# Performance work log

Hardware: AMD Instinct MI355X
Metric: run time of the kernel (lower is better)

## Reference

```python
import jax, jax.numpy as jnp
import numpy as np

N_NODES = 50000
N_EDGES = 800000
IN_DIM = 128
HIDDEN = 16
HEADS1 = 8
OUT_DIM = 128
NEG_SLOPE = 0.2
EPS = 1e-16


def gat_conv(x, src, dst, W, att_src, att_dst, bias, heads, out_ch, concat, num_nodes):
    # x: [N, F_in]; W: [F_in, heads*out_ch]; att_*: [heads, out_ch]; bias: [heads*out_ch] or [out_ch]
    h = (x @ W).reshape(num_nodes, heads, out_ch)          # [N, H, C]
    a_src = jnp.einsum('nhc,hc->nh', h, att_src)           # [N, H]
    a_dst = jnp.einsum('nhc,hc->nh', h, att_dst)           # [N, H]
    alpha = a_src[src] + a_dst[dst]                        # [E, H]
    alpha = jax.nn.leaky_relu(alpha, NEG_SLOPE)
    # segment softmax over incoming edges of each dst node
    amax = jax.ops.segment_max(alpha, dst, num_segments=num_nodes)  # [N, H]
    e = jnp.exp(alpha - amax[dst])                         # [E, H]
    denom = jax.ops.segment_sum(e, dst, num_segments=num_nodes)     # [N, H]
    alpha = e / (denom[dst] + EPS)                         # [E, H]
    msg = h[src] * alpha[:, :, None]                       # [E, H, C]
    out = jax.ops.segment_sum(msg, dst, num_segments=num_nodes)     # [N, H, C]
    if concat:
        out = out.reshape(num_nodes, heads * out_ch)
    else:
        out = out.mean(axis=1)
    return out + bias


def setup_inputs() -> dict:
    key = jax.random.key(0)
    ks = jax.random.split(key, 12)
    x = jax.random.normal(ks[0], (N_NODES, IN_DIM), dtype=jnp.float32)
    edge_index = jax.random.randint(ks[1], (2, N_EDGES), 0, N_NODES, dtype=jnp.int32)
    s1 = 1.0 / np.sqrt(IN_DIM)
    s2 = 1.0 / np.sqrt(HIDDEN * HEADS1)
    W1 = jax.random.normal(ks[2], (IN_DIM, HEADS1 * HIDDEN), dtype=jnp.float32) * s1
    att_src1 = jax.random.normal(ks[3], (HEADS1, HIDDEN), dtype=jnp.float32) * s1
    att_dst1 = jax.random.normal(ks[4], (HEADS1, HIDDEN), dtype=jnp.float32) * s1
    bias1 = jnp.zeros((HEADS1 * HIDDEN,), dtype=jnp.float32)
    W2 = jax.random.normal(ks[5], (HEADS1 * HIDDEN, OUT_DIM), dtype=jnp.float32) * s2
    att_src2 = jax.random.normal(ks[6], (1, OUT_DIM), dtype=jnp.float32) * s2
    att_dst2 = jax.random.normal(ks[7], (1, OUT_DIM), dtype=jnp.float32) * s2
    bias2 = jnp.zeros((OUT_DIM,), dtype=jnp.float32)
    return {"x": x, "edge_index": edge_index,
            "W1": W1, "att_src1": att_src1, "att_dst1": att_dst1, "bias1": bias1,
            "W2": W2, "att_src2": att_src2, "att_dst2": att_dst2, "bias2": bias2}


def reference(x, edge_index, W1, att_src1, att_dst1, bias1, W2, att_src2, att_dst2, bias2):
    # eval mode: F.dropout and attention dropout are identity
    src, dst = edge_index[0], edge_index[1]
    h = gat_conv(x, src, dst, W1, att_src1, att_dst1, bias1,
                 HEADS1, HIDDEN, True, N_NODES)            # [N, HEADS1*HIDDEN]
    h = jax.nn.elu(h)
    out = gat_conv(h, src, dst, W2, att_src2, att_dst2, bias2,
                   1, OUT_DIM, False, N_NODES)             # [N, OUT_DIM]
    return out
```

## Files before the change

### kernel.cpp

```cpp
#include <hip/hip_runtime.h>

#define N_NODES 50000
#define N_EDGES 800000
#define CAP 64
#define NBUCK 196
#define NODES_PAD 50176
#define BBLK 256
#define EPB 3125
#define LOG2E 1.4426950408889634f

typedef unsigned int uint;
typedef unsigned short ushort;
typedef __attribute__((ext_vector_type(2))) float f32x2;
typedef __attribute__((ext_vector_type(4))) float f32x4;
typedef __attribute__((ext_vector_type(8))) short s16x8;

__device__ __forceinline__ f32x2 pk_add(f32x2 a, f32x2 b) {
    f32x2 d;
    asm("v_pk_add_f32 %0, %1, %2" : "=v"(d) : "v"(a), "v"(b));
    return d;
}
__device__ __forceinline__ f32x2 pk_mul(f32x2 a, f32x2 b) {
    f32x2 d;
    asm("v_pk_mul_f32 %0, %1, %2" : "=v"(d) : "v"(a), "v"(b));
    return d;
}
__device__ __forceinline__ f32x2 pk_fma(f32x2 a, f32x2 b, f32x2 c) {
    f32x2 d;
    asm("v_pk_fma_f32 %0, %1, %2, %3" : "=v"(d) : "v"(a), "v"(b), "v"(c));
    return d;
}

__device__ __forceinline__ ushort f2bf(float f) {
    uint u = __float_as_uint(f);
    u = (u + 0x7fffu + ((u >> 16) & 1u)) >> 16;
    return (ushort)u;
}
__device__ __forceinline__ float bf_lo(uint u) { return __uint_as_float(u << 16); }
__device__ __forceinline__ float bf_hi(uint u) { return __uint_as_float(u & 0xffff0000u); }

__global__ __launch_bounds__(256) void bin_count_kernel(
    const int* __restrict__ dstv, uint* __restrict__ counts)
{
    __shared__ uint hist[NBUCK];
    int tid = threadIdx.x, b = blockIdx.x;
    for (int k = tid; k < NBUCK; k += 256) hist[k] = 0;
    __syncthreads();
    int e0 = b * EPB;
    for (int i = tid; i < EPB; i += 256)
        atomicAdd(&hist[((uint)dstv[e0 + i]) >> 8], 1u);
    __syncthreads();
    for (int k = tid; k < NBUCK; k += 256) counts[k * BBLK + b] = hist[k];
}

__global__ __launch_bounds__(256) void scan1_kernel(
    const uint* __restrict__ counts, uint* __restrict__ ofs, uint* __restrict__ bsum)
{
    __shared__ uint wtot[4];
    int tid = threadIdx.x, k = blockIdx.x;
    int lane = tid & 63, wid = tid >> 6;
    uint v = counts[k * 256 + tid];
    uint inc = v;
    #pragma unroll
    for (int o = 1; o < 64; o <<= 1) {
        uint t = __shfl_up(inc, o);
        if (lane >= o) inc += t;
    }
    if (lane == 63) wtot[wid] = inc;
    __syncthreads();
    uint woff = 0;
    for (int w = 0; w < wid; w++) woff += wtot[w];
    uint excl = woff + inc - v;
    ofs[k * 256 + tid] = excl;
    if (tid == 255) bsum[k] = excl + v;
}

__global__ __launch_bounds__(64) void scan2_kernel(
    const uint* __restrict__ bsum, uint* __restrict__ bbase)
{
    int lane = threadIdx.x;
    int base = lane * 4;
    uint v[4];
    #pragma unroll
    for (int j = 0; j < 4; j++) v[j] = (base + j < NBUCK) ? bsum[base + j] : 0u;
    uint s = v[0] + v[1] + v[2] + v[3];
    uint inc = s;
    #pragma unroll
    for (int o = 1; o < 64; o <<= 1) {
        uint t = __shfl_up(inc, o);
        if (lane >= o) inc += t;
    }
    uint run = inc - s;
    #pragma unroll
    for (int j = 0; j < 4; j++) {
        if (base + j < NBUCK) { bbase[base + j] = run; run += v[j]; }
    }
}

__global__ __launch_bounds__(256) void bin_scatter_kernel(
    const int* __restrict__ srcv, const int* __restrict__ dstv,
    const uint* __restrict__ ofs, const uint* __restrict__ bbase,
    uint* __restrict__ binned)
{
    __shared__ uint cur[NBUCK];
    int tid = threadIdx.x, b = blockIdx.x;
    for (int k = tid; k < NBUCK; k += 256) cur[k] = ofs[k * BBLK + b] + bbase[k];
    __syncthreads();
    int e0 = b * EPB;
    for (int i = tid; i < EPB; i += 256) {
        int d = dstv[e0 + i], s = srcv[e0 + i];
        uint k = ((uint)d) >> 8;
        uint pos = atomicAdd(&cur[k], 1u);
        binned[pos] = (((uint)d & 255u) << 16) | (uint)s;
    }
}

__global__ __launch_bounds__(256) void build_kernel(
    const uint* __restrict__ binned, const uint* __restrict__ ofs,
    const uint* __restrict__ bbase,
    int* __restrict__ deg, ushort* __restrict__ list)
{
    __shared__ uint ldeg[256];
    __shared__ ushort llist[256 * CAP];
    int tid = threadIdx.x, k = blockIdx.x;
    ldeg[tid] = 0;
    __syncthreads();
    uint start = ofs[k * 256] + bbase[k];
    uint end = (k == NBUCK - 1) ? N_EDGES : (ofs[(k + 1) * 256] + bbase[k + 1]);
    for (uint i = start + tid; i < end; i += 256) {
        uint p = binned[i];
        uint nl = (p >> 16) & 255u;
        uint slot = atomicAdd(&ldeg[nl], 1u);
        if (slot < CAP) llist[(nl << 6) + slot] = (ushort)(p & 0xFFFFu);
    }
    __syncthreads();
    int node0 = k << 8;
    deg[node0 + tid] = (int)ldeg[tid];
    uint4* d4 = (uint4*)(list + (size_t)node0 * CAP);
    const uint4* s4 = (const uint4*)llist;
    for (int i = tid; i < 256 * CAP * 2 / 16; i += 256) d4[i] = s4[i];
}

__global__ __launch_bounds__(256) void prep_kernel(
    const float* __restrict__ W1, const float* __restrict__ as1, const float* __restrict__ ad1,
    const float* __restrict__ W2, const float* __restrict__ as2, const float* __restrict__ ad2,
    float* __restrict__ WS1, float* __restrict__ WS2)
{
    int idx = blockIdx.x * 256 + threadIdx.x;
    if (idx < 2048) {
        int k = idx >> 4, j = idx & 15;
        const float* att = (j < 8) ? as1 : ad1;
        int head = j & 7;
        float s = 0.f;
        #pragma unroll
        for (int c = 0; c < 16; c++)
            s += W1[k * 128 + head * 16 + c] * att[head * 16 + c];
        WS1[idx] = s * LOG2E;
    } else if (idx < 4096) {
        int idx2 = idx - 2048;
        int k = idx2 >> 4, j = idx2 & 15;
        float s = 0.f;
        if (j < 2) {
            const float* att = j ? ad2 : as2;
            for (int c = 0; c < 128; c++) s += W2[k * 128 + c] * att[c];
        }
        WS2[idx2] = s * LOG2E;
    }
}

template <int HEADS, bool ABF16>
__global__ __launch_bounds__(512) void gemm_mfma_kernel(
    const void* __restrict__ Av, const float* __restrict__ W,
    const float* __restrict__ WS,
    ushort* __restrict__ h16, float* __restrict__ a_src, float* __restrict__ a_dst,
    int nrows)
{
    __shared__ ushort Bf[2304 * 8];
    int tid = threadIdx.x;
    for (int idx = tid; idx < 2304; idx += 512) {
        int t = idx >> 8;
        int rem = idx & 255;
        int kt = rem >> 6, L = rem & 63;
        int col = L & 15;
        int kb = ((L >> 4) << 3) + (kt << 5);
        ushort tmp[8];
        if (t < 8) {
            #pragma unroll
            for (int j = 0; j < 8; j++)
                tmp[j] = f2bf(W[(size_t)(kb + j) * 128 + (t << 4) + col]);
        } else {
            #pragma unroll
            for (int j = 0; j < 8; j++)
                tmp[j] = f2bf(WS[(kb + j) * 16 + col]);
        }
        uint p0 = (uint)tmp[0] | ((uint)tmp[1] << 16);
        uint p1 = (uint)tmp[2] | ((uint)tmp[3] << 16);
        uint p2 = (uint)tmp[4] | ((uint)tmp[5] << 16);
        uint p3 = (uint)tmp[6] | ((uint)tmp[7] << 16);
        *(uint4*)&Bf[idx * 8] = make_uint4(p0, p1, p2, p3);
    }
    __syncthreads();

    int lane = tid & 63;
    int wv = tid >> 6;
    int row0 = (blockIdx.x * 8 + wv) * 16;
    if (row0 >= nrows) return;

    int m = lane & 15, kg = lane >> 4;
    s16x8 afrag[4];
    if (ABF16) {
        const ushort* arow = (const ushort*)Av + (size_t)(row0 + m) * 128 + (kg << 3);
        #pragma unroll
        for (int kt = 0; kt < 4; kt++)
            afrag[kt] = *(const s16x8*)(arow + (kt << 5));
    } else {
        const float* arow = (const float*)Av + (size_t)(row0 + m) * 128 + (kg << 3);
        #pragma unroll
        for (int kt = 0; kt < 4; kt++) {
            float4 f0 = *(const float4*)(arow + (kt << 5));
            float4 f1 = *(const float4*)(arow + (kt << 5) + 4);
            union { s16x8 v; ushort us[8]; } uu;
            uu.us[0] = f2bf(f0.x); uu.us[1] = f2bf(f0.y);
            uu.us[2] = f2bf(f0.z); uu.us[3] = f2bf(f0.w);
            uu.us[4] = f2bf(f1.x); uu.us[5] = f2bf(f1.y);
            uu.us[6] = f2bf(f1.z); uu.us[7] = f2bf(f1.w);
            afrag[kt] = uu.v;
        }
    }

    f32x4 acc[9];
    #pragma unroll
    for (int t = 0; t < 9; t++) acc[t] = (f32x4){0.f, 0.f, 0.f, 0.f};
    #pragma unroll
    for (int t = 0; t < 9; t++) {
        #pragma unroll
        for (int kt = 0; kt < 4; kt++) {
            s16x8 b = *(const s16x8*)&Bf[(((t << 2) + kt) * 64 + lane) * 8];
            acc[t] = __builtin_amdgcn_mfma_f32_16x16x32_bf16(afrag[kt], b, acc[t], 0, 0, 0);
        }
    }

    int colw = lane & 15;
    int rbase = row0 + ((lane >> 4) << 2);
    #pragma unroll
    for (int t = 0; t < 8; t++) {
        #pragma unroll
        for (int r = 0; r < 4; r++)
            h16[(size_t)(rbase + r) * 128 + (t << 4) + colw] = f2bf(acc[t][r]);
    }
    #pragma unroll
    for (int r = 0; r < 4; r++) {
        float v = acc[8][r];
        int row = rbase + r;
        if (HEADS == 8) {
            if (colw < 8) a_src[row * 8 + colw] = v;
            else          a_dst[row * 8 + (colw - 8)] = v;
        } else {
            if (colw == 0)      a_src[row] = v;
            else if (colw == 1) a_dst[row] = v;
        }
    }
}

template <int HEADS, bool ELU, bool OUT16>
__global__ __launch_bounds__(256) void agg_kernel(
    const ushort* __restrict__ h16, const ushort* __restrict__ list,
    const int* __restrict__ deg,
    const float* __restrict__ a_src, const float* __restrict__ a_dst,
    const float* __restrict__ bias, void* __restrict__ outv)
{
    __shared__ float w_lds[4][HEADS][65];
    __shared__ int s_lds[4][64];
    __shared__ float sh_l[4][8];
    int lane = threadIdx.x & 63;
    int wv = threadIdx.x >> 6;
    int n = blockIdx.x * 4 + wv;
    int d = min(deg[n], CAP);
    bool valid = lane < d;
    int s = valid ? (int)list[n * CAP + lane] : 0;
    s_lds[wv][lane] = s << 8;

    if (HEADS == 8) {
        float4 u0 = *(const float4*)&a_src[s * 8];
        float4 u1 = *(const float4*)&a_src[s * 8 + 4];
        float4 v0 = *(const float4*)&a_dst[n * 8];
        float4 v1 = *(const float4*)&a_dst[n * 8 + 4];
        float al[8] = {u0.x + v0.x, u0.y + v0.y, u0.z + v0.z, u0.w + v0.w,
                       u1.x + v1.x, u1.y + v1.y, u1.z + v1.z, u1.w + v1.w};
        float eh[8];
        #pragma unroll
        for (int hh = 0; hh < 8; hh++) {
            float a = fmaxf(al[hh], 0.2f * al[hh]);
            eh[hh] = valid ? exp2f(a) : 0.f;
            w_lds[wv][hh][lane] = eh[hh];
        }
        f32x2 s01 = {eh[0], eh[1]}, s23 = {eh[2], eh[3]};
        f32x2 s45 = {eh[4], eh[5]}, s67 = {eh[6], eh[7]};
        auto lvl = [&](int mm) {
            f32x2 t;
            t.x = __shfl_xor(s01.x, mm); t.y = __shfl_xor(s01.y, mm); s01 = pk_add(s01, t);
            t.x = __shfl_xor(s23.x, mm); t.y = __shfl_xor(s23.y, mm); s23 = pk_add(s23, t);
            t.x = __shfl_xor(s45.x, mm); t.y = __shfl_xor(s45.y, mm); s45 = pk_add(s45, t);
            t.x = __shfl_xor(s67.x, mm); t.y = __shfl_xor(s67.y, mm); s67 = pk_add(s67, t);
        };
        lvl(1); lvl(2); lvl(4); lvl(8);
        if (d > 16) lvl(16);
        if (d > 32) lvl(32);
        if (lane == 0) {
            *(f32x2*)&sh_l[wv][0] = s01; *(f32x2*)&sh_l[wv][2] = s23;
            *(f32x2*)&sh_l[wv][4] = s45; *(f32x2*)&sh_l[wv][6] = s67;
        }
    } else {
        float a = a_src[s] + a_dst[n];
        a = fmaxf(a, 0.2f * a);
        float eh0 = valid ? exp2f(a) : 0.f;
        w_lds[wv][0][lane] = eh0;
        float sh = eh0;
        sh += __shfl_xor(sh, 1); sh += __shfl_xor(sh, 2);
        sh += __shfl_xor(sh, 4); sh += __shfl_xor(sh, 8);
        if (d > 16) sh += __shfl_xor(sh, 16);
        if (d > 32) sh += __shfl_xor(sh, 32);
        if (lane == 0) sh_l[wv][0] = sh;
    }

    int half = lane >> 5;
    int lq = lane & 31;
    int c0 = lq << 2;
    int g = (HEADS == 8) ? (lq >> 2) : 0;
    const char* hp = (const char*)h16 + (c0 << 1);
    f32x2 acc01 = {0.f, 0.f}, acc23 = {0.f, 0.f};
    int d8 = (d + 7) & ~7;
    for (int e0 = 0; e0 < d8; e0 += 8) {
        int soff[4]; float wv4[4]; uint2 u[4];
        #pragma unroll
        for (int r = 0; r < 4; r++) {
            int e = e0 + (r << 1) + half;
            soff[r] = s_lds[wv][e];
            wv4[r] = w_lds[wv][g][e];
        }
        #pragma unroll
        for (int r = 0; r < 4; r++)
            u[r] = *(const uint2*)(hp + soff[r]);
        #pragma unroll
        for (int r = 0; r < 4; r++) {
            f32x2 wp = {wv4[r], wv4[r]};
            f32x2 lo = {bf_lo(u[r].x), bf_hi(u[r].x)};
            f32x2 hi = {bf_lo(u[r].y), bf_hi(u[r].y)};
            acc01 = pk_fma(wp, lo, acc01);
            acc23 = pk_fma(wp, hi, acc23);
        }
    }
    f32x2 t;
    t.x = __shfl_xor(acc01.x, 32); t.y = __shfl_xor(acc01.y, 32); acc01 = pk_add(acc01, t);
    t.x = __shfl_xor(acc23.x, 32); t.y = __shfl_xor(acc23.y, 32); acc23 = pk_add(acc23, t);

    float shv = sh_l[wv][g];
    float r = __builtin_amdgcn_rcpf(shv + 1e-16f);
    f32x2 rr = {r, r};
    acc01 = pk_mul(acc01, rr);
    acc23 = pk_mul(acc23, rr);
    float4 bv = *(const float4*)&bias[c0];
    float o0 = acc01.x + bv.x, o1 = acc01.y + bv.y;
    float o2 = acc23.x + bv.z, o3 = acc23.y + bv.w;
    if (ELU) {
        o0 = o0 > 0.f ? o0 : __expf(o0) - 1.f;
        o1 = o1 > 0.f ? o1 : __expf(o1) - 1.f;
        o2 = o2 > 0.f ? o2 : __expf(o2) - 1.f;
        o3 = o3 > 0.f ? o3 : __expf(o3) - 1.f;
    }
    if (lane < 32) {
        if (OUT16) {
            uint2 pk;
            pk.x = (uint)f2bf(o0) | ((uint)f2bf(o1) << 16);
            pk.y = (uint)f2bf(o2) | ((uint)f2bf(o3) << 16);
            *(uint2*)((ushort*)outv + (size_t)n * 128 + c0) = pk;
        } else {
            *(float4*)((float*)outv + (size_t)n * 128 + c0) = make_float4(o0, o1, o2, o3);
        }
    }
}

extern "C" void kernel_launch(void* const* d_in, const int* in_sizes, int n_in,
                              void* d_out, int out_size, void* d_ws, size_t ws_size,
                              hipStream_t stream)
{
    (void)in_sizes; (void)n_in; (void)out_size; (void)ws_size;
    const float* x   = (const float*)d_in[0];
    const int*   ei  = (const int*)d_in[1];
    const float* W1  = (const float*)d_in[2];
    const float* as1 = (const float*)d_in[3];
    const float* ad1 = (const float*)d_in[4];
    const float* b1  = (const float*)d_in[5];
    const float* W2  = (const float*)d_in[6];
    const float* as2 = (const float*)d_in[7];
    const float* ad2 = (const float*)d_in[8];
    const float* b2  = (const float*)d_in[9];
    float* out = (float*)d_out;
    const int* srcv = ei;
    const int* dstv = ei + N_EDGES;

    char* ws = (char*)d_ws;
    size_t off = 0;
    auto alloc = [&](size_t bytes) {
        void* p = ws + off;
        off += (bytes + 255) & ~(size_t)255;
        return p;
    };
    ushort* h1_16 = (ushort*)alloc((size_t)N_NODES * 128 * 2);
    ushort* h2_16 = (ushort*)alloc((size_t)N_NODES * 128 * 2);
    ushort* h1b   = (ushort*)alloc((size_t)N_NODES * 128 * 2);
    float*  asrc1 = (float*)alloc((size_t)N_NODES * 8 * 4);
    float*  adst1 = (float*)alloc((size_t)N_NODES * 8 * 4);
    float*  asrc2 = (float*)alloc((size_t)N_NODES * 4);
    float*  adst2 = (float*)alloc((size_t)N_NODES * 4);
    int*    degp  = (int*)alloc((size_t)NODES_PAD * 4);
    ushort* list  = (ushort*)alloc((size_t)NODES_PAD * CAP * 2);
    float*  WS1   = (float*)alloc(128 * 16 * 4);
    float*  WS2   = (float*)alloc(128 * 16 * 4);
    uint* binned = (uint*)h1b;
    uint* counts = binned + N_EDGES;
    uint* ofsp   = counts + NODES_PAD;
    uint* bsum   = ofsp + NODES_PAD;
    uint* bbase  = bsum + NBUCK;

    const int NG = (N_NODES + 3) / 4;
    const int GB = (N_NODES / 16 + 7) / 8;

    prep_kernel<<<16, 256, 0, stream>>>(W1, as1, ad1, W2, as2, ad2, WS1, WS2);
    bin_count_kernel<<<BBLK, 256, 0, stream>>>(dstv, counts);
    scan1_kernel<<<NBUCK, 256, 0, stream>>>(counts, ofsp, bsum);
    scan2_kernel<<<1, 64, 0, stream>>>(bsum, bbase);
    bin_scatter_kernel<<<BBLK, 256, 0, stream>>>(srcv, dstv, ofsp, bbase, binned);
    build_kernel<<<NBUCK, 256, 0, stream>>>(binned, ofsp, bbase, degp, list);

    gemm_mfma_kernel<8, false><<<GB, 512, 0, stream>>>(x, W1, WS1, h1_16, asrc1, adst1, N_NODES);
    agg_kernel<8, true, true><<<NG, 256, 0, stream>>>(h1_16, list, degp, asrc1, adst1, b1, h1b);

    gemm_mfma_kernel<1, true><<<GB, 512, 0, stream>>>(h1b, W2, WS2, h2_16, asrc2, adst2, N_NODES);
    agg_kernel<1, false, false><<<NG, 256, 0, stream>>>(h2_16, list, degp, asrc2, adst2, b2, out);
}
```

Before: 125.5 us.

## Split aggregation across channel groups, shrink build buckets, merge prep into scan2

The aggregation kernel now launches four blocks per node group, each handling 32 channels (two heads), and normalizes attention weights before accumulation. This spreads the gather work over more waves and trims the LDS per-head weight table. Binning now uses 64-node buckets (782 of them) so each build block needs less LDS and more blocks run in parallel. The prep kernel is folded into the scan2 launch to save one launch. More blocks re-read the neighbor lists and attention logits, and there are more scan1 blocks. With N_NODES/4*4 blocks the last grid covers exactly 50000 nodes.

```diff
diff --git a/kernel.cpp b/kernel.cpp
--- a/kernel.cpp
+++ b/kernel.cpp
@@ -3,8 +3,8 @@
 #define N_NODES 50000
 #define N_EDGES 800000
 #define CAP 64
-#define NBUCK 196
-#define NODES_PAD 50176
+#define NBUCK 782
+#define NODES_PAD 50048
 #define BBLK 256
 #define EPB 3125
 #define LOG2E 1.4426950408889634f
@@ -20,11 +20,6 @@
     asm("v_pk_add_f32 %0, %1, %2" : "=v"(d) : "v"(a), "v"(b));
     return d;
 }
-__device__ __forceinline__ f32x2 pk_mul(f32x2 a, f32x2 b) {
-    f32x2 d;
-    asm("v_pk_mul_f32 %0, %1, %2" : "=v"(d) : "v"(a), "v"(b));
-    return d;
-}
 __device__ __forceinline__ f32x2 pk_fma(f32x2 a, f32x2 b, f32x2 c) {
     f32x2 d;
     asm("v_pk_fma_f32 %0, %1, %2, %3" : "=v"(d) : "v"(a), "v"(b), "v"(c));
@@ -48,7 +43,7 @@
     __syncthreads();
     int e0 = b * EPB;
     for (int i = tid; i < EPB; i += 256)
-        atomicAdd(&hist[((uint)dstv[e0 + i]) >> 8], 1u);
+        atomicAdd(&hist[((uint)dstv[e0 + i]) >> 6], 1u);
     __syncthreads();
     for (int k = tid; k < NBUCK; k += 256) counts[k * BBLK + b] = hist[k];
 }
@@ -75,25 +70,58 @@
     if (tid == 255) bsum[k] = excl + v;
 }
 
-__global__ __launch_bounds__(64) void scan2_kernel(
-    const uint* __restrict__ bsum, uint* __restrict__ bbase)
-{
-    int lane = threadIdx.x;
-    int base = lane * 4;
-    uint v[4];
-    #pragma unroll
-    for (int j = 0; j < 4; j++) v[j] = (base + j < NBUCK) ? bsum[base + j] : 0u;
-    uint s = v[0] + v[1] + v[2] + v[3];
-    uint inc = s;
-    #pragma unroll
-    for (int o = 1; o < 64; o <<= 1) {
-        uint t = __shfl_up(inc, o);
-        if (lane >= o) inc += t;
-    }
-    uint run = inc - s;
-    #pragma unroll
-    for (int j = 0; j < 4; j++) {
-        if (base + j < NBUCK) { bbase[base + j] = run; run += v[j]; }
+__global__ __launch_bounds__(256) void scan2_prep_kernel(
+    const uint* __restrict__ bsum, uint* __restrict__ bbase,
+    const float* __restrict__ W1, const float* __restrict__ as1, const float* __restrict__ ad1,
+    const float* __restrict__ W2, const float* __restrict__ as2, const float* __restrict__ ad2,
+    float* __restrict__ WS1, float* __restrict__ WS2)
+{
+    int bid = blockIdx.x;
+    int tid = threadIdx.x;
+    if (bid == 0) {
+        __shared__ uint wtot[4];
+        int lane = tid & 63, wid = tid >> 6;
+        int base = tid * 4;
+        uint v[4];
+        #pragma unroll
+        for (int j = 0; j < 4; j++) v[j] = (base + j < NBUCK) ? bsum[base + j] : 0u;
+        uint s = v[0] + v[1] + v[2] + v[3];
+        uint inc = s;
+        #pragma unroll
+        for (int o = 1; o < 64; o <<= 1) {
+            uint t = __shfl_up(inc, o);
+            if (lane >= o) inc += t;
+        }
+        if (lane == 63) wtot[wid] = inc;
+        __syncthreads();
+        uint woff = 0;
+        for (int w = 0; w < wid; w++) woff += wtot[w];
+        uint run = woff + inc - s;
+        #pragma unroll
+        for (int j = 0; j < 4; j++) {
+            if (base + j < NBUCK) { bbase[base + j] = run; run += v[j]; }
+        }
+    } else {
+        int idx = (bid - 1) * 256 + tid;
+        if (idx < 2048) {
+            int k = idx >> 4, j = idx & 15;
+            const float* att = (j < 8) ? as1 : ad1;
+            int head = j & 7;
+            float s = 0.f;
+            #pragma unroll
+            for (int c = 0; c < 16; c++)
+                s += W1[k * 128 + head * 16 + c] * att[head * 16 + c];
+            WS1[idx] = s * LOG2E;
+        } else {
+            int idx2 = idx - 2048;
+            int k = idx2 >> 4, j = idx2 & 15;
+            float s = 0.f;
+            if (j < 2) {
+                const float* att = j ? ad2 : as2;
+                for (int c = 0; c < 128; c++) s += W2[k * 128 + c] * att[c];
+            }
+            WS2[idx2] = s * LOG2E;
+        }
     }
 }
 
@@ -109,9 +137,9 @@
     int e0 = b * EPB;
     for (int i = tid; i < EPB; i += 256) {
         int d = dstv[e0 + i], s = srcv[e0 + i];
-        uint k = ((uint)d) >> 8;
+        uint k = ((uint)d) >> 6;
         uint pos = atomicAdd(&cur[k], 1u);
-        binned[pos] = (((uint)d & 255u) << 16) | (uint)s;
+        binned[pos] = (((uint)d & 63u) << 16) | (uint)s;
     }
 }
 
@@ -120,52 +148,25 @@
     const uint* __restrict__ bbase,
     int* __restrict__ deg, ushort* __restrict__ list)
 {
-    __shared__ uint ldeg[256];
-    __shared__ ushort llist[256 * CAP];
+    __shared__ uint ldeg[64];
+    __shared__ ushort llist[64 * CAP];
     int tid = threadIdx.x, k = blockIdx.x;
-    ldeg[tid] = 0;
+    if (tid < 64) ldeg[tid] = 0;
     __syncthreads();
     uint start = ofs[k * 256] + bbase[k];
     uint end = (k == NBUCK - 1) ? N_EDGES : (ofs[(k + 1) * 256] + bbase[k + 1]);
     for (uint i = start + tid; i < end; i += 256) {
         uint p = binned[i];
-        uint nl = (p >> 16) & 255u;
+        uint nl = (p >> 16) & 63u;
         uint slot = atomicAdd(&ldeg[nl], 1u);
         if (slot < CAP) llist[(nl << 6) + slot] = (ushort)(p & 0xFFFFu);
     }
     __syncthreads();
-    int node0 = k << 8;
-    deg[node0 + tid] = (int)ldeg[tid];
+    int node0 = k << 6;
+    if (tid < 64) deg[node0 + tid] = (int)ldeg[tid];
     uint4* d4 = (uint4*)(list + (size_t)node0 * CAP);
     const uint4* s4 = (const uint4*)llist;
-    for (int i = tid; i < 256 * CAP * 2 / 16; i += 256) d4[i] = s4[i];
-}
-
-__global__ __launch_bounds__(256) void prep_kernel(
-    const float* __restrict__ W1, const float* __restrict__ as1, const float* __restrict__ ad1,
-    const float* __restrict__ W2, const float* __restrict__ as2, const float* __restrict__ ad2,
-    float* __restrict__ WS1, float* __restrict__ WS2)
-{
-    int idx = blockIdx.x * 256 + threadIdx.x;
-    if (idx < 2048) {
-        int k = idx >> 4, j = idx & 15;
-        const float* att = (j < 8) ? as1 : ad1;
-        int head = j & 7;
-        float s = 0.f;
-        #pragma unroll
-        for (int c = 0; c < 16; c++)
-            s += W1[k * 128 + head * 16 + c] * att[head * 16 + c];
-        WS1[idx] = s * LOG2E;
-    } else if (idx < 4096) {
-        int idx2 = idx - 2048;
-        int k = idx2 >> 4, j = idx2 & 15;
-        float s = 0.f;
-        if (j < 2) {
-            const float* att = j ? ad2 : as2;
-            for (int c = 0; c < 128; c++) s += W2[k * 128 + c] * att[c];
-        }
-        WS2[idx2] = s * LOG2E;
-    }
+    for (int i = tid; i < 64 * CAP * 2 / 16; i += 256) d4[i] = s4[i];
 }
 
 template <int HEADS, bool ABF16>
@@ -269,113 +270,99 @@
     const float* __restrict__ a_src, const float* __restrict__ a_dst,
     const float* __restrict__ bias, void* __restrict__ outv)
 {
-    __shared__ float w_lds[4][HEADS][65];
+    __shared__ float w_lds[4][2][64];
     __shared__ int s_lds[4][64];
-    __shared__ float sh_l[4][8];
+    int bid = blockIdx.x;
+    int cg = bid & 3;
     int lane = threadIdx.x & 63;
     int wv = threadIdx.x >> 6;
-    int n = blockIdx.x * 4 + wv;
+    int n = (bid >> 2) * 4 + wv;
     int d = min(deg[n], CAP);
     bool valid = lane < d;
     int s = valid ? (int)list[n * CAP + lane] : 0;
-    s_lds[wv][lane] = s << 8;
+    s_lds[wv][lane] = (s << 8) + (cg << 6);
 
     if (HEADS == 8) {
-        float4 u0 = *(const float4*)&a_src[s * 8];
-        float4 u1 = *(const float4*)&a_src[s * 8 + 4];
-        float4 v0 = *(const float4*)&a_dst[n * 8];
-        float4 v1 = *(const float4*)&a_dst[n * 8 + 4];
-        float al[8] = {u0.x + v0.x, u0.y + v0.y, u0.z + v0.z, u0.w + v0.w,
-                       u1.x + v1.x, u1.y + v1.y, u1.z + v1.z, u1.w + v1.w};
-        float eh[8];
-        #pragma unroll
-        for (int hh = 0; hh < 8; hh++) {
-            float a = fmaxf(al[hh], 0.2f * al[hh]);
-            eh[hh] = valid ? exp2f(a) : 0.f;
-            w_lds[wv][hh][lane] = eh[hh];
-        }
-        f32x2 s01 = {eh[0], eh[1]}, s23 = {eh[2], eh[3]};
-        f32x2 s45 = {eh[4], eh[5]}, s67 = {eh[6], eh[7]};
-        auto lvl = [&](int mm) {
-            f32x2 t;
-            t.x = __shfl_xor(s01.x, mm); t.y = __shfl_xor(s01.y, mm); s01 = pk_add(s01, t);
-            t.x = __shfl_xor(s23.x, mm); t.y = __shfl_xor(s23.y, mm); s23 = pk_add(s23, t);
-            t.x = __shfl_xor(s45.x, mm); t.y = __shfl_xor(s45.y, mm); s45 = pk_add(s45, t);
-            t.x = __shfl_xor(s67.x, mm); t.y = __shfl_xor(s67.y, mm); s67 = pk_add(s67, t);
-        };
-        lvl(1); lvl(2); lvl(4); lvl(8);
-        if (d > 16) lvl(16);
-        if (d > 32) lvl(32);
-        if (lane == 0) {
-            *(f32x2*)&sh_l[wv][0] = s01; *(f32x2*)&sh_l[wv][2] = s23;
-            *(f32x2*)&sh_l[wv][4] = s45; *(f32x2*)&sh_l[wv][6] = s67;
-        }
+        float2 us = *(const float2*)&a_src[s * 8 + 2 * cg];
+        float2 ud = *(const float2*)&a_dst[n * 8 + 2 * cg];
+        float a0 = us.x + ud.x, a1 = us.y + ud.y;
+        a0 = fmaxf(a0, 0.2f * a0);
+        a1 = fmaxf(a1, 0.2f * a1);
+        float e0 = valid ? exp2f(a0) : 0.f;
+        float e1 = valid ? exp2f(a1) : 0.f;
+        f32x2 ss = {e0, e1};
+        #pragma unroll
+        for (int mm = 1; mm < 16; mm <<= 1) {
+            f32x2 t; t.x = __shfl_xor(ss.x, mm); t.y = __shfl_xor(ss.y, mm);
+            ss = pk_add(ss, t);
+        }
+        if (d > 16) { f32x2 t; t.x = __shfl_xor(ss.x, 16); t.y = __shfl_xor(ss.y, 16); ss = pk_add(ss, t); }
+        if (d > 32) { f32x2 t; t.x = __shfl_xor(ss.x, 32); t.y = __shfl_xor(ss.y, 32); ss = pk_add(ss, t); }
+        w_lds[wv][0][lane] = e0 * __builtin_amdgcn_rcpf(ss.x + 1e-16f);
+        w_lds[wv][1][lane] = e1 * __builtin_amdgcn_rcpf(ss.y + 1e-16f);
     } else {
         float a = a_src[s] + a_dst[n];
         a = fmaxf(a, 0.2f * a);
-        float eh0 = valid ? exp2f(a) : 0.f;
-        w_lds[wv][0][lane] = eh0;
-        float sh = eh0;
+        float e0 = valid ? exp2f(a) : 0.f;
+        float sh = e0;
         sh += __shfl_xor(sh, 1); sh += __shfl_xor(sh, 2);
         sh += __shfl_xor(sh, 4); sh += __shfl_xor(sh, 8);
         if (d > 16) sh += __shfl_xor(sh, 16);
         if (d > 32) sh += __shfl_xor(sh, 32);
-        if (lane == 0) sh_l[wv][0] = sh;
-    }
-
-    int half = lane >> 5;
-    int lq = lane & 31;
-    int c0 = lq << 2;
-    int g = (HEADS == 8) ? (lq >> 2) : 0;
-    const char* hp = (const char*)h16 + (c0 << 1);
+        float w = e0 * __builtin_amdgcn_rcpf(sh + 1e-16f);
+        w_lds[wv][0][lane] = w;
+        w_lds[wv][1][lane] = w;
+    }
+
+    int eg = lane >> 3;
+    int lq = lane & 7;
+    int hsel = lq >> 2;
+    const char* hp = (const char*)h16 + (lq << 3);
+    uint2 u[8];
+    float wk[8];
+    #pragma unroll
+    for (int t = 0; t < 8; t++) {
+        if ((t << 3) < d) {
+            int e = (t << 3) + eg;
+            u[t] = *(const uint2*)(hp + s_lds[wv][e]);
+            wk[t] = w_lds[wv][hsel][e];
+        }
+    }
     f32x2 acc01 = {0.f, 0.f}, acc23 = {0.f, 0.f};
-    int d8 = (d + 7) & ~7;
-    for (int e0 = 0; e0 < d8; e0 += 8) {
-        int soff[4]; float wv4[4]; uint2 u[4];
-        #pragma unroll
-        for (int r = 0; r < 4; r++) {
-            int e = e0 + (r << 1) + half;
-            soff[r] = s_lds[wv][e];
-            wv4[r] = w_lds[wv][g][e];
-        }
-        #pragma unroll
-        for (int r = 0; r < 4; r++)
-            u[r] = *(const uint2*)(hp + soff[r]);
-        #pragma unroll
-        for (int r = 0; r < 4; r++) {
-            f32x2 wp = {wv4[r], wv4[r]};
-            f32x2 lo = {bf_lo(u[r].x), bf_hi(u[r].x)};
-            f32x2 hi = {bf_lo(u[r].y), bf_hi(u[r].y)};
+    #pragma unroll
+    for (int t = 0; t < 8; t++) {
+        if ((t << 3) < d) {
+            f32x2 wp = {wk[t], wk[t]};
+            f32x2 lo = {bf_lo(u[t].x), bf_hi(u[t].x)};
+            f32x2 hi = {bf_lo(u[t].y), bf_hi(u[t].y)};
             acc01 = pk_fma(wp, lo, acc01);
             acc23 = pk_fma(wp, hi, acc23);
         }
     }
-    f32x2 t;
-    t.x = __shfl_xor(acc01.x, 32); t.y = __shfl_xor(acc01.y, 32); acc01 = pk_add(acc01, t);
-    t.x = __shfl_xor(acc23.x, 32); t.y = __shfl_xor(acc23.y, 32); acc23 = pk_add(acc23, t);
-
-    float shv = sh_l[wv][g];
-    float r = __builtin_amdgcn_rcpf(shv + 1e-16f);
-    f32x2 rr = {r, r};
-    acc01 = pk_mul(acc01, rr);
-    acc23 = pk_mul(acc23, rr);
-    float4 bv = *(const float4*)&bias[c0];
-    float o0 = acc01.x + bv.x, o1 = acc01.y + bv.y;
-    float o2 = acc23.x + bv.z, o3 = acc23.y + bv.w;
-    if (ELU) {
-        o0 = o0 > 0.f ? o0 : __expf(o0) - 1.f;
-        o1 = o1 > 0.f ? o1 : __expf(o1) - 1.f;
-        o2 = o2 > 0.f ? o2 : __expf(o2) - 1.f;
-        o3 = o3 > 0.f ? o3 : __expf(o3) - 1.f;
-    }
-    if (lane < 32) {
+    #pragma unroll
+    for (int mm = 8; mm < 64; mm <<= 1) {
+        f32x2 t;
+        t.x = __shfl_xor(acc01.x, mm); t.y = __shfl_xor(acc01.y, mm); acc01 = pk_add(acc01, t);
+        t.x = __shfl_xor(acc23.x, mm); t.y = __shfl_xor(acc23.y, mm); acc23 = pk_add(acc23, t);
+    }
+    if (lane < 8) {
+        int ch = (cg << 5) + (lq << 2);
+        float4 bv = *(const float4*)&bias[ch];
+        float o0 = acc01.x + bv.x, o1 = acc01.y + bv.y;
+        float o2 = acc23.x + bv.z, o3 = acc23.y + bv.w;
+        if (ELU) {
+            o0 = o0 > 0.f ? o0 : __expf(o0) - 1.f;
+            o1 = o1 > 0.f ? o1 : __expf(o1) - 1.f;
+            o2 = o2 > 0.f ? o2 : __expf(o2) - 1.f;
+            o3 = o3 > 0.f ? o3 : __expf(o3) - 1.f;
+        }
         if (OUT16) {
             uint2 pk;
             pk.x = (uint)f2bf(o0) | ((uint)f2bf(o1) << 16);
             pk.y = (uint)f2bf(o2) | ((uint)f2bf(o3) << 16);
-            *(uint2*)((ushort*)outv + (size_t)n * 128 + c0) = pk;
+            *(uint2*)((ushort*)outv + (size_t)n * 128 + ch) = pk;
         } else {
-            *(float4*)((float*)outv + (size_t)n * 128 + c0) = make_float4(o0, o1, o2, o3);
+            *(float4*)((float*)outv + (size_t)n * 128 + ch) = make_float4(o0, o1, o2, o3);
         }
     }
 }
@@ -419,23 +406,22 @@
     float*  WS2   = (float*)alloc(128 * 16 * 4);
     uint* binned = (uint*)h1b;
     uint* counts = binned + N_EDGES;
-    uint* ofsp   = counts + NODES_PAD;
-    uint* bsum   = ofsp + NODES_PAD;
+    uint* ofsp   = counts + NBUCK * BBLK;
+    uint* bsum   = ofsp + NBUCK * BBLK;
     uint* bbase  = bsum + NBUCK;
 
-    const int NG = (N_NODES + 3) / 4;
+    const int AG = (N_NODES / 4) * 4;
     const int GB = (N_NODES / 16 + 7) / 8;
 
-    prep_kernel<<<16, 256, 0, stream>>>(W1, as1, ad1, W2, as2, ad2, WS1, WS2);
     bin_count_kernel<<<BBLK, 256, 0, stream>>>(dstv, counts);
     scan1_kernel<<<NBUCK, 256, 0, stream>>>(counts, ofsp, bsum);
-    scan2_kernel<<<1, 64, 0, stream>>>(bsum, bbase);
+    scan2_prep_kernel<<<17, 256, 0, stream>>>(bsum, bbase, W1, as1, ad1, W2, as2, ad2, WS1, WS2);
     bin_scatter_kernel<<<BBLK, 256, 0, stream>>>(srcv, dstv, ofsp, bbase, binned);
     build_kernel<<<NBUCK, 256, 0, stream>>>(binned, ofsp, bbase, degp, list);
 
     gemm_mfma_kernel<8, false><<<GB, 512, 0, stream>>>(x, W1, WS1, h1_16, asrc1, adst1, N_NODES);
-    agg_kernel<8, true, true><<<NG, 256, 0, stream>>>(h1_16, list, degp, asrc1, adst1, b1, h1b);
+    agg_kernel<8, true, true><<<AG, 256, 0, stream>>>(h1_16, list, degp, asrc1, adst1, b1, h1b);
 
     gemm_mfma_kernel<1, true><<<GB, 512, 0, stream>>>(h1b, W2, WS2, h2_16, asrc2, adst2, N_NODES);
-    agg_kernel<1, false, false><<<NG, 256, 0, stream>>>(h2_16, list, degp, asrc2, adst2, b2, out);
-}
+    agg_kernel<1, false, false><<<AG, 256, 0, stream>>>(h2_16, list, degp, asrc2, adst2, b2, out);
+}
```

Result: slower. 208.7 us (+66.3%).
